# Kernel tuning notes

Hardware: AMD Instinct MI355X
Metric: run time of the kernel (lower is better)

The kernel has to match this reference:

```python
import jax, jax.numpy as jnp
import numpy as np

N = 12288      # number of nodes
D = 256        # in_features
K = 31         # k_neighbours + 1
EPS = 1e-12    # F.normalize eps


def setup_inputs() -> dict:
    key = jax.random.key(0)
    k1, k2, k3 = jax.random.split(key, 3)
    x = jax.random.normal(k1, (N, D), dtype=jnp.float32)
    # Attentive layer params: elementwise feature weights (torch init is ones;
    # perturb so the reference is non-degenerate)
    w0 = 1.0 + 0.1 * jax.random.normal(k2, (D,), dtype=jnp.float32)
    w1 = 1.0 + 0.1 * jax.random.normal(k3, (D,), dtype=jnp.float32)
    return {"x": x, "w0": w0, "w1": w1}


def reference(x, w0, w1):
    # internal_forward: relu(Attentive_0(x)) then Attentive_1 (last layer, no act)
    h = jax.nn.relu(x * w0)          # [N, D]
    h = h * w1                        # [N, D]
    # F.normalize(dim=-1, p=2)
    norm = jnp.sqrt(jnp.sum(h * h, axis=-1, keepdims=True))
    h = h / jnp.maximum(norm, EPS)
    # cal_similarity_graph: dense NxN similarity
    s = jnp.einsum('nd,md->nm', h, h)  # [N, N]
    # graph_top_K: keep top-K entries per row, zero the rest (scatter mask)
    _, idx = jax.lax.top_k(s, K)       # idx: [N, K]
    rows = jnp.arange(s.shape[0])[:, None]
    mask = jnp.zeros_like(s).at[rows, idx].set(1.0)
    # apply_non_linearity 'relu'
    return jax.nn.relu(s * mask)
```

## Files before the change

### kernel.cpp

```cpp
#include <hip/hip_runtime.h>
#include <cstdint>
#include <cstddef>
#include <math.h>

#define N_NODES 12288
#define D_FEAT  256
#define K_TOP   31

typedef float nfloat4 __attribute__((ext_vector_type(4)));

__device__ __forceinline__ float np_g(float xv, float w0v, float w1v) {
  #pragma clang fp contract(off)
  float t = __fmul_rn(xv, w0v);
  t = fmaxf(t, 0.0f);
  return __fmul_rn(t, w1v);
}

__device__ __forceinline__ void nt_store4(float* p, float4 v) {
  nfloat4 nv;
  nv.x = v.x; nv.y = v.y; nv.z = v.z; nv.w = v.w;
  __builtin_nontemporal_store(nv, reinterpret_cast<nfloat4*>(p));
}

__global__ __launch_bounds__(256) void np_norm_kernel(
    const float* __restrict__ x, const float* __restrict__ w0,
    const float* __restrict__ w1, float* __restrict__ nrm) {
  #pragma clang fp contract(off)
  const int n = blockIdx.x * blockDim.x + threadIdx.x;
  if (n >= N_NODES) return;
  const float* xr = x + (size_t)n * D_FEAT;
  float blk[2];
  #pragma unroll
  for (int b = 0; b < 2; ++b) {
    float r[8];
    #pragma unroll
    for (int j = 0; j < 8; ++j) {
      const int d = 128 * b + j;
      const float g = np_g(xr[d], w0[d], w1[d]);
      r[j] = __fmul_rn(g, g);
    }
    for (int i = 8; i < 128; i += 8) {
      #pragma unroll
      for (int j = 0; j < 8; ++j) {
        const int d = 128 * b + i + j;
        const float g = np_g(xr[d], w0[d], w1[d]);
        r[j] = __fadd_rn(r[j], __fmul_rn(g, g));
      }
    }
    blk[b] = __fadd_rn(
        __fadd_rn(__fadd_rn(r[0], r[1]), __fadd_rn(r[2], r[3])),
        __fadd_rn(__fadd_rn(r[4], r[5]), __fadd_rn(r[6], r[7])));
  }
  const float tot = __fadd_rn(blk[0], blk[1]);
  nrm[n] = fmaxf(__fsqrt_rn(tot), 1e-12f);
}

__global__ __launch_bounds__(256) void np_h_kernel(
    const float* __restrict__ x, const float* __restrict__ w0,
    const float* __restrict__ w1, const float* __restrict__ nrm,
    float* __restrict__ h) {
  #pragma clang fp contract(off)
  const int q = blockIdx.x * blockDim.x + threadIdx.x;
  const int base = q * 4;
  if (base >= N_NODES * D_FEAT) return;
  const int n = base >> 8;
  const int d = base & (D_FEAT - 1);
  const float ia = nrm[n];
  const float4 xv = *reinterpret_cast<const float4*>(&x[base]);
  const float4 w0v = *reinterpret_cast<const float4*>(&w0[d]);
  const float4 w1v = *reinterpret_cast<const float4*>(&w1[d]);
  float4 o;
  o.x = __fdiv_rn(np_g(xv.x, w0v.x, w1v.x), ia);
  o.y = __fdiv_rn(np_g(xv.y, w0v.y, w1v.y), ia);
  o.z = __fdiv_rn(np_g(xv.z, w0v.z, w1v.z), ia);
  o.w = __fdiv_rn(np_g(xv.w, w0v.w, w1v.w), ia);
  *reinterpret_cast<float4*>(&h[base]) = o;
}

#define BT 128
#define BK 32
#define TBW 132
#define NTILES (N_NODES / BT)
#define NBLOCKS (NTILES * (NTILES + 1) / 2)

template <int PRE>
__global__ __launch_bounds__(256, 2) void np_gemm_kernel(
    const float* __restrict__ x, const float* __restrict__ w0,
    const float* __restrict__ w1, const float* __restrict__ nrm,
    const float* __restrict__ h, float* __restrict__ out) {
  #pragma clang fp contract(off)
  __shared__ __align__(16) float smem[64 * TBW];
  float (*As)[BT] = reinterpret_cast<float (*)[BT]>(smem);
  float (*Bs)[BT] = reinterpret_cast<float (*)[BT]>(smem + BK * BT);
  float (*tb)[TBW] = reinterpret_cast<float (*)[TBW]>(smem);

  const int L = blockIdx.x;
  int by = (int)(96.5 - sqrt(96.5 * 96.5 - 2.0 * (double)L));
  while (by > 0 && by * NTILES - by * (by - 1) / 2 > L) --by;
  while ((by + 1) * NTILES - (by + 1) * by / 2 <= L) ++by;
  const int bx = by + (L - (by * NTILES - by * (by - 1) / 2));

  const int n0 = by * BT;
  const int m0 = bx * BT;
  const int t = threadIdx.x;
  const int tx = t & 15, ty = t >> 4;
  const int sr = t >> 1;
  const int sk = (t & 1) * 16;

  float acc[8][8] = {};

  for (int k0 = 0; k0 < D_FEAT; k0 += BK) {
    __syncthreads();
    if (PRE) {
      #pragma unroll
      for (int q = 0; q < 4; ++q) {
        const int c = sk + q * 4;
        const float4 ha = *reinterpret_cast<const float4*>(
            &h[(size_t)(n0 + sr) * D_FEAT + k0 + c]);
        const float4 hb = *reinterpret_cast<const float4*>(
            &h[(size_t)(m0 + sr) * D_FEAT + k0 + c]);
        As[c + 0][sr] = ha.x; As[c + 1][sr] = ha.y;
        As[c + 2][sr] = ha.z; As[c + 3][sr] = ha.w;
        Bs[c + 0][sr] = hb.x; Bs[c + 1][sr] = hb.y;
        Bs[c + 2][sr] = hb.z; Bs[c + 3][sr] = hb.w;
      }
    } else {
      const float ia = nrm[n0 + sr];
      const float ib = nrm[m0 + sr];
      #pragma unroll
      for (int q = 0; q < 4; ++q) {
        const int c = sk + q * 4;
        const float4 xa = *reinterpret_cast<const float4*>(
            &x[(size_t)(n0 + sr) * D_FEAT + k0 + c]);
        const float4 xb = *reinterpret_cast<const float4*>(
            &x[(size_t)(m0 + sr) * D_FEAT + k0 + c]);
        const float4 wa = *reinterpret_cast<const float4*>(&w0[k0 + c]);
        const float4 wb = *reinterpret_cast<const float4*>(&w1[k0 + c]);
        const float xaf[4] = {xa.x, xa.y, xa.z, xa.w};
        const float xbf[4] = {xb.x, xb.y, xb.z, xb.w};
        const float w0f[4] = {wa.x, wa.y, wa.z, wa.w};
        const float w1f[4] = {wb.x, wb.y, wb.z, wb.w};
        #pragma unroll
        for (int e = 0; e < 4; ++e) {
          As[c + e][sr] = __fdiv_rn(np_g(xaf[e], w0f[e], w1f[e]), ia);
          Bs[c + e][sr] = __fdiv_rn(np_g(xbf[e], w0f[e], w1f[e]), ib);
        }
      }
    }
    __syncthreads();

    for (int kk = 0; kk < BK; ++kk) {
      const float4 a0 = *reinterpret_cast<const float4*>(&As[kk][ty * 4]);
      const float4 a1 = *reinterpret_cast<const float4*>(&As[kk][64 + ty * 4]);
      const float4 b0 = *reinterpret_cast<const float4*>(&Bs[kk][tx * 4]);
      const float4 b1 = *reinterpret_cast<const float4*>(&Bs[kk][64 + tx * 4]);
      const float af[8] = {a0.x, a0.y, a0.z, a0.w, a1.x, a1.y, a1.z, a1.w};
      const float bf[8] = {b0.x, b0.y, b0.z, b0.w, b1.x, b1.y, b1.z, b1.w};
      #pragma unroll
      for (int i = 0; i < 8; ++i)
        #pragma unroll
        for (int j = 0; j < 8; ++j)
          acc[i][j] = __builtin_fmaf(af[i], bf[j], acc[i][j]);
    }
  }

  #pragma unroll
  for (int i = 0; i < 8; ++i) {
    const int row = n0 + (i >> 2) * 64 + ty * 4 + (i & 3);
    float4 o0, o1;
    o0.x = acc[i][0]; o0.y = acc[i][1]; o0.z = acc[i][2]; o0.w = acc[i][3];
    o1.x = acc[i][4]; o1.y = acc[i][5]; o1.z = acc[i][6]; o1.w = acc[i][7];
    nt_store4(&out[(size_t)row * N_NODES + m0 + tx * 4], o0);
    nt_store4(&out[(size_t)row * N_NODES + m0 + 64 + tx * 4], o1);
  }

  if (bx != by) {
    #pragma unroll
    for (int hh = 0; hh < 2; ++hh) {
      __syncthreads();
      #pragma unroll
      for (int r = 0; r < 4; ++r) {
        const int j = hh * 4 + r;
        const int ml = tx * 4 + r;
        #pragma unroll
        for (int ih = 0; ih < 2; ++ih) {
          float4 v;
          v.x = acc[ih * 4 + 0][j];
          v.y = acc[ih * 4 + 1][j];
          v.z = acc[ih * 4 + 2][j];
          v.w = acc[ih * 4 + 3][j];
          *reinterpret_cast<float4*>(&tb[ml][ih * 64 + ty * 4]) = v;
        }
      }
      __syncthreads();
      #pragma unroll
      for (int p = 0; p < 8; ++p) {
        const int row = (t >> 5) + 8 * p;
        const int col = (t & 31) * 4;
        const float4 v = *reinterpret_cast<const float4*>(&tb[row][col]);
        nt_store4(&out[(size_t)(m0 + hh * 64 + row) * N_NODES + n0 + col], v);
      }
    }
  }
}

__device__ inline float att_decode(unsigned uu) {
  return (uu & 0x80000000u) ? __uint_as_float(uu & 0x7FFFFFFFu)
                            : __uint_as_float(~uu);
}

#define HBINS 2048

__global__ __launch_bounds__(256) void att_topk_kernel(float* __restrict__ s) {
  const int n = blockIdx.x;
  float* row = s + (size_t)n * N_NODES;
  const int t = threadIdx.x;
  const int lane = t & 63, wid = t >> 6;

  unsigned u[48];
#pragma unroll
  for (int i = 0; i < 12; ++i) {
    float4 v = reinterpret_cast<const float4*>(row)[t + 256 * i];
    const float f[4] = {v.x, v.y, v.z, v.w};
#pragma unroll
    for (int j = 0; j < 4; ++j) {
      unsigned b = __float_as_uint(f[j]);
      u[i * 4 + j] = (b & 0x80000000u) ? ~b : (b | 0x80000000u);
    }
  }

  __shared__ unsigned hist[HBINS];
  __shared__ unsigned wmn[4], wmx[4];
  __shared__ int wred[4];
  __shared__ unsigned bc_mn, bc_mx, bc_T;
  __shared__ int bc_B, bc_above, bc_cnt, bc_cand;
  __shared__ int cnt_s;

  unsigned mymn = u[0], mymx = u[0];
#pragma unroll
  for (int i = 1; i < 48; ++i) {
    mymn = u[i] < mymn ? u[i] : mymn;
    mymx = u[i] > mymx ? u[i] : mymx;
  }
#pragma unroll
  for (int o = 32; o > 0; o >>= 1) {
    const unsigned a = __shfl_down(mymn, o);
    const unsigned b = __shfl_down(mymx, o);
    mymn = a < mymn ? a : mymn;
    mymx = b > mymx ? b : mymx;
  }
  if (lane == 0) { wmn[wid] = mymn; wmx[wid] = mymx; }
  __syncthreads();
  if (t == 0) {
    unsigned mn = wmn[0], mx = wmx[0];
    for (int w = 1; w < 4; ++w) {
      mn = wmn[w] < mn ? wmn[w] : mn;
      mx = wmx[w] > mx ? wmx[w] : mx;
    }
    bc_mn = mn; bc_mx = mx;
  }
  __syncthreads();

  unsigned T;
  if (bc_mn == bc_mx) {
    T = bc_mn;
  } else {
    unsigned cur_lo = bc_mn;
    unsigned cur_range = bc_mx - bc_mn;
    int above_total = 0;
    bool done = false;
    for (int pass = 0; pass < 4 && !done; ++pass) {
      const int bits = 32 - __clz(cur_range);
      const int sh = bits > 11 ? bits - 11 : 0;
#pragma unroll
      for (int q = 0; q < HBINS / 256; ++q) hist[t + 256 * q] = 0u;
      __syncthreads();
#pragma unroll
      for (int i = 0; i < 48; ++i) {
        const unsigned rel = u[i] - cur_lo;
        if (u[i] >= cur_lo && rel <= cur_range)
          atomicAdd(&hist[rel >> sh], 1u);
      }
      __syncthreads();
      int hloc[8];
      int part = 0;
#pragma unroll
      for (int q = 0; q < 8; ++q) { hloc[q] = (int)hist[8 * t + q]; part += hloc[q]; }
      int v = part;
#pragma unroll
      for (int o = 1; o < 64; o <<= 1) {
        const int z = __shfl_down(v, o);
        if (lane + o < 64) v += z;
      }
      if (lane == 0) wred[wid] = v;
      __syncthreads();
      int wsuf = 0;
      for (int w = wid + 1; w < 4; ++w) wsuf += wred[w];
      const int suffix_incl = v + wsuf;
      int run = suffix_incl - part;
      int fB = -1, fAbove = 0, fCnt = 0;
#pragma unroll
      for (int q = 7; q >= 0; --q) {
        const int above = run;
        const int cnt = hloc[q];
        if (cnt > 0 && above_total + above < K_TOP &&
            above_total + above + cnt >= K_TOP) {
          fB = 8 * t + q; fAbove = above; fCnt = cnt;
        }
        run += cnt;
      }
      if (fB >= 0) { bc_B = fB; bc_above = fAbove; bc_cnt = fCnt; }
      __syncthreads();
      const int B = bc_B;
      const int aboveB = bc_above;
      const int cntB = bc_cnt;
      const unsigned bin_lo = cur_lo + ((unsigned)B << sh);
      if (sh == 0) {
        T = bin_lo;
        done = true;
      } else if (cntB <= HBINS) {
        if (t == 0) bc_cand = 0;
        __syncthreads();
#pragma unroll
        for (int i = 0; i < 48; ++i) {
          const unsigned rel = u[i] - cur_lo;
          if (u[i] >= cur_lo && rel <= cur_range && (int)(rel >> sh) == B) {
            const int slot = atomicAdd(&bc_cand, 1);
            hist[slot] = u[i];
          }
        }
        __syncthreads();
        const int m = bc_cand;
        const int kb = K_TOP - above_total - aboveB;
        for (int e = t; e < m; e += 256) {
          const unsigned ce = hist[e];
          int gt = 0, eq = 0;
          for (int e2 = 0; e2 < m; ++e2) {
            const unsigned c2 = hist[e2];
            gt += (c2 > ce) ? 1 : 0;
            eq += (c2 == ce) ? 1 : 0;
          }
          if (gt < kb && gt + eq >= kb) bc_T = ce;
        }
        __syncthreads();
        T = bc_T;
        done = true;
      } else {
        above_total += aboveB;
        cur_lo = bin_lo;
        cur_range = (1u << sh) - 1u;
      }
      __syncthreads();
    }
  }

  {
    int cg = 0, ce = 0;
#pragma unroll
    for (int i = 0; i < 48; ++i) {
      cg += (u[i] > T) ? 1 : 0;
      ce += (u[i] == T) ? 1 : 0;
    }
    int packed = (cg << 16) | ce;
#pragma unroll
    for (int o = 32; o > 0; o >>= 1) packed += __shfl_down(packed, o);
    if (t == 0) cnt_s = 0;
    __syncthreads();
    if ((t & 63) == 0) atomicAdd(&cnt_s, packed);
    __syncthreads();
  }
  const int tot = cnt_s;
  __syncthreads();
  const int tot_gt = tot >> 16;
  const int tot_eq = tot & 0xFFFF;
  const int need = K_TOP - tot_gt;

  if (tot_eq == need) {
#pragma unroll
    for (int i = 0; i < 12; ++i) {
      float vals[4];
#pragma unroll
      for (int j = 0; j < 4; ++j) {
        const unsigned uu = u[i * 4 + j];
        const float f = att_decode(uu);
        vals[j] = (uu >= T) ? fmaxf(f, 0.0f) : 0.0f;
      }
      float4 o; o.x = vals[0]; o.y = vals[1]; o.z = vals[2]; o.w = vals[3];
      reinterpret_cast<float4*>(row)[t + 256 * i] = o;
    }
  } else {
    __shared__ int eqc[12][256];
#pragma unroll
    for (int i = 0; i < 12; ++i) {
      int c = 0;
#pragma unroll
      for (int j = 0; j < 4; ++j) c += (u[i * 4 + j] == T) ? 1 : 0;
      eqc[i][t] = c;
    }
    __syncthreads();
    int base[12];
    {
      int run = 0;
      for (int i = 0; i < 12; ++i) {
        int pre = 0, tt_tot = 0;
        for (int tt = 0; tt < 256; ++tt) {
          const int vv = eqc[i][tt];
          if (tt < t) pre += vv;
          tt_tot += vv;
        }
        base[i] = run + pre;
        run += tt_tot;
      }
    }
#pragma unroll
    for (int i = 0; i < 12; ++i) {
      float vals[4];
      int r = base[i];
#pragma unroll
      for (int j = 0; j < 4; ++j) {
        const unsigned uu = u[i * 4 + j];
        const float f = att_decode(uu);
        bool keep = false;
        if (uu > T) keep = true;
        else if (uu == T) { keep = (r < need); ++r; }
        vals[j] = keep ? fmaxf(f, 0.0f) : 0.0f;
      }
      float4 o; o.x = vals[0]; o.y = vals[1]; o.z = vals[2]; o.w = vals[3];
      reinterpret_cast<float4*>(row)[t + 256 * i] = o;
    }
  }
}

extern "C" void kernel_launch(void* const* d_in, const int* in_sizes, int n_in,
                              void* d_out, int out_size, void* d_ws, size_t ws_size,
                              hipStream_t stream) {
  const float* x  = (const float*)d_in[0];
  const float* w0 = (const float*)d_in[1];
  const float* w1 = (const float*)d_in[2];
  float* out = (float*)d_out;
  float* nrm = (float*)d_ws;
  float* h = (float*)((char*)d_ws + 65536);

  const size_t need = 65536 + (size_t)N_NODES * D_FEAT * 4;

  np_norm_kernel<<<N_NODES / 256, 256, 0, stream>>>(x, w0, w1, nrm);

  if (ws_size >= need) {
    np_h_kernel<<<(N_NODES * D_FEAT / 4 + 255) / 256, 256, 0, stream>>>(
        x, w0, w1, nrm, h);
    np_gemm_kernel<1><<<NBLOCKS, 256, 0, stream>>>(x, w0, w1, nrm, h, out);
  } else {
    np_gemm_kernel<0><<<NBLOCKS, 256, 0, stream>>>(x, w0, w1, nrm, nullptr, out);
  }

  att_topk_kernel<<<N_NODES, 256, 0, stream>>>(out);
}
```

Baseline: 701.6 us.

## Store normalized features transposed so GEMM tiles load with vector LDS stores

The precompute kernel now writes h in transposed [D, N] layout through a padded shared-memory tile. The GEMM loads each K-slice row directly as float4 into padded As/Bs arrays, replacing the scalar transposing LDS stores. The shared arrays now use a padded row width of 132. The GEMM launch bound also rises from 2 to 3 blocks per CU, which may cap registers for the 8x8 accumulator and risk spills.

New measurement: 712.8 us. About the same (+1.6%).

```diff
diff --git a/kernel.cpp b/kernel.cpp
--- a/kernel.cpp
+++ b/kernel.cpp
@@ -55,44 +55,61 @@
   nrm[n] = fmaxf(__fsqrt_rn(tot), 1e-12f);
 }
 
-__global__ __launch_bounds__(256) void np_h_kernel(
+__global__ __launch_bounds__(256) void np_hT_kernel(
     const float* __restrict__ x, const float* __restrict__ w0,
     const float* __restrict__ w1, const float* __restrict__ nrm,
-    float* __restrict__ h) {
+    float* __restrict__ hT) {
   #pragma clang fp contract(off)
-  const int q = blockIdx.x * blockDim.x + threadIdx.x;
-  const int base = q * 4;
-  if (base >= N_NODES * D_FEAT) return;
-  const int n = base >> 8;
-  const int d = base & (D_FEAT - 1);
+  __shared__ float tile[64][65];
+  const int tn0 = (blockIdx.x % 192) * 64;
+  const int td0 = (blockIdx.x / 192) * 64;
+  const int t = threadIdx.x;
+  const int lr = t >> 2;
+  const int cg = (t & 3) * 16;
+  const int n = tn0 + lr;
   const float ia = nrm[n];
-  const float4 xv = *reinterpret_cast<const float4*>(&x[base]);
-  const float4 w0v = *reinterpret_cast<const float4*>(&w0[d]);
-  const float4 w1v = *reinterpret_cast<const float4*>(&w1[d]);
-  float4 o;
-  o.x = __fdiv_rn(np_g(xv.x, w0v.x, w1v.x), ia);
-  o.y = __fdiv_rn(np_g(xv.y, w0v.y, w1v.y), ia);
-  o.z = __fdiv_rn(np_g(xv.z, w0v.z, w1v.z), ia);
-  o.w = __fdiv_rn(np_g(xv.w, w0v.w, w1v.w), ia);
-  *reinterpret_cast<float4*>(&h[base]) = o;
+  #pragma unroll
+  for (int q = 0; q < 4; ++q) {
+    const int dl = cg + q * 4;
+    const int d = td0 + dl;
+    const float4 xv = *reinterpret_cast<const float4*>(&x[(size_t)n * D_FEAT + d]);
+    const float4 w0v = *reinterpret_cast<const float4*>(&w0[d]);
+    const float4 w1v = *reinterpret_cast<const float4*>(&w1[d]);
+    tile[dl + 0][lr] = __fdiv_rn(np_g(xv.x, w0v.x, w1v.x), ia);
+    tile[dl + 1][lr] = __fdiv_rn(np_g(xv.y, w0v.y, w1v.y), ia);
+    tile[dl + 2][lr] = __fdiv_rn(np_g(xv.z, w0v.z, w1v.z), ia);
+    tile[dl + 3][lr] = __fdiv_rn(np_g(xv.w, w0v.w, w1v.w), ia);
+  }
+  __syncthreads();
+  const int dr = t >> 2;
+  #pragma unroll
+  for (int q = 0; q < 4; ++q) {
+    const int nl = (t & 3) * 16 + q * 4;
+    float4 o;
+    o.x = tile[dr][nl + 0];
+    o.y = tile[dr][nl + 1];
+    o.z = tile[dr][nl + 2];
+    o.w = tile[dr][nl + 3];
+    *reinterpret_cast<float4*>(&hT[(size_t)(td0 + dr) * N_NODES + tn0 + nl]) = o;
+  }
 }
 
 #define BT 128
 #define BK 32
-#define TBW 132
+#define SLDW 132
 #define NTILES (N_NODES / BT)
 #define NBLOCKS (NTILES * (NTILES + 1) / 2)
 
 template <int PRE>
-__global__ __launch_bounds__(256, 2) void np_gemm_kernel(
+__global__ __launch_bounds__(256, 3) void np_gemm_kernel(
     const float* __restrict__ x, const float* __restrict__ w0,
     const float* __restrict__ w1, const float* __restrict__ nrm,
-    const float* __restrict__ h, float* __restrict__ out) {
+    const float* __restrict__ hT, float* __restrict__ out) {
   #pragma clang fp contract(off)
-  __shared__ __align__(16) float smem[64 * TBW];
-  float (*As)[BT] = reinterpret_cast<float (*)[BT]>(smem);
-  float (*Bs)[BT] = reinterpret_cast<float (*)[BT]>(smem + BK * BT);
-  float (*tb)[TBW] = reinterpret_cast<float (*)[TBW]>(smem);
+  __shared__ __align__(16) float smem[64 * SLDW];
+  float (*As)[SLDW] = reinterpret_cast<float (*)[SLDW]>(smem);
+  float (*Bs)[SLDW] = reinterpret_cast<float (*)[SLDW]>(smem + BK * SLDW);
+  float (*tb)[SLDW] = reinterpret_cast<float (*)[SLDW]>(smem);
 
   const int L = blockIdx.x;
   int by = (int)(96.5 - sqrt(96.5 * 96.5 - 2.0 * (double)L));
@@ -104,27 +121,27 @@
   const int m0 = bx * BT;
   const int t = threadIdx.x;
   const int tx = t & 15, ty = t >> 4;
-  const int sr = t >> 1;
-  const int sk = (t & 1) * 16;
+  const int kr = t >> 3;
+  const int cb = (t & 7) * 16;
 
   float acc[8][8] = {};
 
   for (int k0 = 0; k0 < D_FEAT; k0 += BK) {
     __syncthreads();
     if (PRE) {
-      #pragma unroll
-      for (int q = 0; q < 4; ++q) {
-        const int c = sk + q * 4;
-        const float4 ha = *reinterpret_cast<const float4*>(
-            &h[(size_t)(n0 + sr) * D_FEAT + k0 + c]);
-        const float4 hb = *reinterpret_cast<const float4*>(
-            &h[(size_t)(m0 + sr) * D_FEAT + k0 + c]);
-        As[c + 0][sr] = ha.x; As[c + 1][sr] = ha.y;
-        As[c + 2][sr] = ha.z; As[c + 3][sr] = ha.w;
-        Bs[c + 0][sr] = hb.x; Bs[c + 1][sr] = hb.y;
-        Bs[c + 2][sr] = hb.z; Bs[c + 3][sr] = hb.w;
-      }
+      const float* ha = &hT[(size_t)(k0 + kr) * N_NODES + n0 + cb];
+      const float* hb = &hT[(size_t)(k0 + kr) * N_NODES + m0 + cb];
+      #pragma unroll
+      for (int q = 0; q < 4; ++q)
+        *reinterpret_cast<float4*>(&As[kr][cb + q * 4]) =
+            *reinterpret_cast<const float4*>(&ha[q * 4]);
+      #pragma unroll
+      for (int q = 0; q < 4; ++q)
+        *reinterpret_cast<float4*>(&Bs[kr][cb + q * 4]) =
+            *reinterpret_cast<const float4*>(&hb[q * 4]);
     } else {
+      const int sr = t >> 1;
+      const int sk = (t & 1) * 16;
       const float ia = nrm[n0 + sr];
       const float ib = nrm[m0 + sr];
       #pragma unroll
@@ -439,16 +456,15 @@
   const float* w1 = (const float*)d_in[2];
   float* out = (float*)d_out;
   float* nrm = (float*)d_ws;
-  float* h = (float*)((char*)d_ws + 65536);
+  float* hT = (float*)((char*)d_ws + 65536);
 
   const size_t need = 65536 + (size_t)N_NODES * D_FEAT * 4;
 
   np_norm_kernel<<<N_NODES / 256, 256, 0, stream>>>(x, w0, w1, nrm);
 
   if (ws_size >= need) {
-    np_h_kernel<<<(N_NODES * D_FEAT / 4 + 255) / 256, 256, 0, stream>>>(
-        x, w0, w1, nrm, h);
-    np_gemm_kernel<1><<<NBLOCKS, 256, 0, stream>>>(x, w0, w1, nrm, h, out);
+    np_hT_kernel<<<192 * (D_FEAT / 64), 256, 0, stream>>>(x, w0, w1, nrm, hT);
+    np_gemm_kernel<1><<<NBLOCKS, 256, 0, stream>>>(x, w0, w1, nrm, hT, out);
   } else {
     np_gemm_kernel<0><<<NBLOCKS, 256, 0, stream>>>(x, w0, w1, nrm, nullptr, out);
   }
```

## Prefetch next K-slice of normalized features into registers during GEMM compute

Applied to the files above, without the earlier changes.

In the precomputed-h path of the similarity GEMM, the next BK slice of A and B rows is loaded into registers while the current slice is used for FMAs from shared memory. Barriers become raw s_barrier calls with explicit lgkmcnt waits, so global load latency is no longer waited on before the barrier. Launch bounds rise from 2 to 3 blocks per CU, which tightens the register budget while the prefetch buffers add register pressure, with a risk of spills.

Result: slower. 719.8 us (+2.6%).

```diff
diff --git a/kernel.cpp b/kernel.cpp
--- a/kernel.cpp
+++ b/kernel.cpp
@@ -84,7 +84,7 @@
 #define NBLOCKS (NTILES * (NTILES + 1) / 2)
 
 template <int PRE>
-__global__ __launch_bounds__(256, 2) void np_gemm_kernel(
+__global__ __launch_bounds__(256, 3) void np_gemm_kernel(
     const float* __restrict__ x, const float* __restrict__ w0,
     const float* __restrict__ w1, const float* __restrict__ nrm,
     const float* __restrict__ h, float* __restrict__ out) {
@@ -109,22 +109,55 @@
 
   float acc[8][8] = {};
 
-  for (int k0 = 0; k0 < D_FEAT; k0 += BK) {
-    __syncthreads();
-    if (PRE) {
+  if (PRE) {
+    float4 ra[4], rb[4];
+    const float* hA = &h[(size_t)(n0 + sr) * D_FEAT + sk];
+    const float* hB = &h[(size_t)(m0 + sr) * D_FEAT + sk];
+    #pragma unroll
+    for (int q = 0; q < 4; ++q) {
+      ra[q] = *reinterpret_cast<const float4*>(&hA[q * 4]);
+      rb[q] = *reinterpret_cast<const float4*>(&hB[q * 4]);
+    }
+
+    #pragma unroll
+    for (int k0 = 0; k0 < D_FEAT; k0 += BK) {
       #pragma unroll
       for (int q = 0; q < 4; ++q) {
         const int c = sk + q * 4;
-        const float4 ha = *reinterpret_cast<const float4*>(
-            &h[(size_t)(n0 + sr) * D_FEAT + k0 + c]);
-        const float4 hb = *reinterpret_cast<const float4*>(
-            &h[(size_t)(m0 + sr) * D_FEAT + k0 + c]);
-        As[c + 0][sr] = ha.x; As[c + 1][sr] = ha.y;
-        As[c + 2][sr] = ha.z; As[c + 3][sr] = ha.w;
-        Bs[c + 0][sr] = hb.x; Bs[c + 1][sr] = hb.y;
-        Bs[c + 2][sr] = hb.z; Bs[c + 3][sr] = hb.w;
-      }
-    } else {
+        As[c + 0][sr] = ra[q].x; As[c + 1][sr] = ra[q].y;
+        As[c + 2][sr] = ra[q].z; As[c + 3][sr] = ra[q].w;
+        Bs[c + 0][sr] = rb[q].x; Bs[c + 1][sr] = rb[q].y;
+        Bs[c + 2][sr] = rb[q].z; Bs[c + 3][sr] = rb[q].w;
+      }
+      if (k0 + BK < D_FEAT) {
+        #pragma unroll
+        for (int q = 0; q < 4; ++q) {
+          ra[q] = *reinterpret_cast<const float4*>(&hA[k0 + BK + q * 4]);
+          rb[q] = *reinterpret_cast<const float4*>(&hB[k0 + BK + q * 4]);
+        }
+      }
+      asm volatile("s_waitcnt lgkmcnt(0)" ::: "memory");
+      __builtin_amdgcn_s_barrier();
+
+      for (int kk = 0; kk < BK; ++kk) {
+        const float4 a0 = *reinterpret_cast<const float4*>(&As[kk][ty * 4]);
+        const float4 a1 = *reinterpret_cast<const float4*>(&As[kk][64 + ty * 4]);
+        const float4 b0 = *reinterpret_cast<const float4*>(&Bs[kk][tx * 4]);
+        const float4 b1 = *reinterpret_cast<const float4*>(&Bs[kk][64 + tx * 4]);
+        const float af[8] = {a0.x, a0.y, a0.z, a0.w, a1.x, a1.y, a1.z, a1.w};
+        const float bf[8] = {b0.x, b0.y, b0.z, b0.w, b1.x, b1.y, b1.z, b1.w};
+        #pragma unroll
+        for (int i = 0; i < 8; ++i)
+          #pragma unroll
+          for (int j = 0; j < 8; ++j)
+            acc[i][j] = __builtin_fmaf(af[i], bf[j], acc[i][j]);
+      }
+      asm volatile("s_waitcnt lgkmcnt(0)" ::: "memory");
+      __builtin_amdgcn_s_barrier();
+    }
+  } else {
+    for (int k0 = 0; k0 < D_FEAT; k0 += BK) {
+      __syncthreads();
       const float ia = nrm[n0 + sr];
       const float ib = nrm[m0 + sr];
       #pragma unroll
@@ -146,22 +179,22 @@
           Bs[c + e][sr] = __fdiv_rn(np_g(xbf[e], w0f[e], w1f[e]), ib);
         }
       }
+      __syncthreads();
+      for (int kk = 0; kk < BK; ++kk) {
+        const float4 a0 = *reinterpret_cast<const float4*>(&As[kk][ty * 4]);
+        const float4 a1 = *reinterpret_cast<const float4*>(&As[kk][64 + ty * 4]);
+        const float4 b0 = *reinterpret_cast<const float4*>(&Bs[kk][tx * 4]);
+        const float4 b1 = *reinterpret_cast<const float4*>(&Bs[kk][64 + tx * 4]);
+        const float af[8] = {a0.x, a0.y, a0.z, a0.w, a1.x, a1.y, a1.z, a1.w};
+        const float bf[8] = {b0.x, b0.y, b0.z, b0.w, b1.x, b1.y, b1.z, b1.w};
+        #pragma unroll
+        for (int i = 0; i < 8; ++i)
+          #pragma unroll
+          for (int j = 0; j < 8; ++j)
+            acc[i][j] = __builtin_fmaf(af[i], bf[j], acc[i][j]);
+      }
     }
     __syncthreads();
-
-    for (int kk = 0; kk < BK; ++kk) {
-      const float4 a0 = *reinterpret_cast<const float4*>(&As[kk][ty * 4]);
-      const float4 a1 = *reinterpret_cast<const float4*>(&As[kk][64 + ty * 4]);
-      const float4 b0 = *reinterpret_cast<const float4*>(&Bs[kk][tx * 4]);
-      const float4 b1 = *reinterpret_cast<const float4*>(&Bs[kk][64 + tx * 4]);
-      const float af[8] = {a0.x, a0.y, a0.z, a0.w, a1.x, a1.y, a1.z, a1.w};
-      const float bf[8] = {b0.x, b0.y, b0.z, b0.w, b1.x, b1.y, b1.z, b1.w};
-      #pragma unroll
-      for (int i = 0; i < 8; ++i)
-        #pragma unroll
-        for (int j = 0; j < 8; ++j)
-          acc[i][j] = __builtin_fmaf(af[i], bf[j], acc[i][j]);
-    }
   }
 
   #pragma unroll
```
